# Performance work log

Hardware: AMD Instinct MI355X
Metric: run time of the kernel (lower is better)

The kernel has to match this reference:

```python
import jax, jax.numpy as jnp
import numpy as np

B, P, O, C = 32, 65536, 32, 2
THRESH = 0.35
VAR = (0.1, 0.2)
LOC_W, LANDM_W = 2.0, 1.0
ALPHA, GAMMA = 0.25, 1.5
EPS = 1e-7


def setup_inputs():
    key = jax.random.key(0)
    k = jax.random.split(key, 8)
    loc_data = jax.random.normal(k[0], (B, P, 4), jnp.float32) * 0.1
    conf_data = jax.random.normal(k[1], (B, P, C), jnp.float32)
    landm_data = jax.random.normal(k[2], (B, P, 10), jnp.float32) * 0.1
    # priors in center form (cx, cy, w, h)
    cxcy = jax.random.uniform(k[3], (P, 2), minval=0.05, maxval=0.95)
    wh = jax.random.uniform(k[4], (P, 2), minval=0.02, maxval=0.3)
    priors = jnp.concatenate([cxcy, wh], axis=-1).astype(jnp.float32)
    # targets [B, O, 15]: corner box (4) + 5 landmarks (10) + label (1, in {-1, +1})
    xy1 = jax.random.uniform(k[5], (B, O, 2), minval=0.0, maxval=0.7)
    bwh = jax.random.uniform(k[6], (B, O, 2), minval=0.05, maxval=0.25)
    boxes = jnp.concatenate([xy1, xy1 + bwh], axis=-1)
    landms = jnp.tile(xy1 + bwh * 0.5, (1, 1, 5))
    labels = (jax.random.randint(k[7], (B, O, 1), 0, 2) * 2 - 1).astype(jnp.float32)
    targets = jnp.concatenate([boxes, landms, labels], axis=-1)
    return {"loc_data": loc_data, "conf_data": conf_data, "landm_data": landm_data,
            "priors": priors, "targets": targets}


def point_form(pr):  # (cx,cy,w,h) -> (x1,y1,x2,y2)
    return jnp.concatenate([pr[:, :2] - pr[:, 2:] / 2, pr[:, :2] + pr[:, 2:] / 2], -1)


def pairwise_iou(a, b):  # a [O,4], b [P,4] corner form -> [O,P]
    lt = jnp.maximum(a[:, None, :2], b[None, :, :2])
    rb = jnp.minimum(a[:, None, 2:], b[None, :, 2:])
    whd = jnp.clip(rb - lt, 0.0)
    inter = whd[..., 0] * whd[..., 1]
    area_a = ((a[:, 2] - a[:, 0]) * (a[:, 3] - a[:, 1]))[:, None]
    area_b = ((b[:, 2] - b[:, 0]) * (b[:, 3] - b[:, 1]))[None, :]
    return inter / (area_a + area_b - inter)


def encode_landm(matched, priors):  # matched [P,10], priors [P,4] center form
    m = matched.reshape(P, 5, 2)
    g = (m - priors[:, None, :2]) / (VAR[0] * priors[:, None, 2:])
    return g.reshape(P, 10)


def match_one(truths, landms, labels, priors_pf, priors):
    ov = pairwise_iou(truths, priors_pf)                       # [O,P]
    best_prior_idx = jnp.argmax(ov, axis=1)                    # [O] best prior per gt
    best_truth_overlap = ov.max(axis=0)                        # [P]
    best_truth_idx = jnp.argmax(ov, axis=0)                    # [P]
    # ensure every gt keeps its best prior
    best_truth_overlap = best_truth_overlap.at[best_prior_idx].set(2.0)
    best_truth_idx = best_truth_idx.at[best_prior_idx].set(jnp.arange(truths.shape[0]))
    loc_t = truths[best_truth_idx]                             # [P,4] matched gt boxes (corner)
    conf = jnp.where(best_truth_overlap < THRESH, 0.0, labels[best_truth_idx])
    landm_t = encode_landm(landms[best_truth_idx], priors)     # [P,10]
    return loc_t, conf, landm_t


def decode(loc, priors):  # SSD center-form decode -> corner boxes
    xy = priors[..., :2] + loc[..., :2] * VAR[0] * priors[..., 2:]
    wh = priors[..., 2:] * jnp.exp(loc[..., 2:] * VAR[1])
    return jnp.concatenate([xy - wh / 2, xy + wh / 2], -1)


def giou(b1, b2):  # elementwise GIoU, corner form
    area1 = (b1[..., 2] - b1[..., 0]) * (b1[..., 3] - b1[..., 1])
    area2 = (b2[..., 2] - b2[..., 0]) * (b2[..., 3] - b2[..., 1])
    iw = jnp.clip(jnp.minimum(b1[..., 2], b2[..., 2]) - jnp.maximum(b1[..., 0], b2[..., 0]), 0.0)
    ih = jnp.clip(jnp.minimum(b1[..., 3], b2[..., 3]) - jnp.maximum(b1[..., 1], b2[..., 1]), 0.0)
    inter = iw * ih
    union = area1 + area2 - inter
    iou = inter / (union + EPS)
    ew = jnp.maximum(b1[..., 2], b2[..., 2]) - jnp.minimum(b1[..., 0], b2[..., 0])
    eh = jnp.maximum(b1[..., 3], b2[..., 3]) - jnp.minimum(b1[..., 1], b2[..., 1])
    enc = ew * eh
    return iou - (enc - union) / (enc + EPS)


def smooth_l1(x):
    ax = jnp.abs(x)
    return jnp.where(ax < 1.0, 0.5 * x * x, ax - 0.5)


def reference(loc_data, conf_data, landm_data, priors, targets):
    # matching uses detached (.data) priors/targets in the original
    priors_c = jax.lax.stop_gradient(priors)
    targets_c = jax.lax.stop_gradient(targets)
    truths, landms, labels = targets_c[..., :4], targets_c[..., 4:14], targets_c[..., 14]
    priors_pf = point_form(priors_c)
    loc_t, conf_raw, landm_t = jax.vmap(match_one, in_axes=(0, 0, 0, None, None))(
        truths, landms, labels, priors_pf, priors_c)  # [B,P,4],[B,P],[B,P,10]

    # landmark loss on pos1 = conf > 0 (label +1: face with landmarks)
    pos1 = conf_raw > 0
    N1 = jnp.maximum(pos1.sum().astype(jnp.float32), 1.0)
    loss_landm = (smooth_l1(landm_data - landm_t).sum(-1) * pos1).sum() * LANDM_W

    # loc GIoU loss on pos = conf != 0
    pos = conf_raw != 0
    conf_t = pos.astype(jnp.int32)  # conf_t[pos] = 1, background 0
    dec = decode(loc_data, priors_c[None])  # [B,P,4]
    loss_l = jnp.where(pos, 1.0 - giou(dec, loc_t), 0.0).sum() * LOC_W

    # focal loss over all B*P anchors (size_average=False -> sum)
    logp = jax.nn.log_softmax(conf_data, axis=-1)
    logp_t = jnp.take_along_axis(logp, conf_t[..., None], axis=-1)[..., 0]
    p_t = jnp.exp(logp_t)
    loss_c = (-ALPHA * (1.0 - p_t) ** GAMMA * logp_t).sum()

    # original normalizes loss_l and loss_c by num_pos_landm sum (N), landm by N1 (==N)
    N = N1
    return (loss_l / N, loss_c / N, loss_landm / N1)
```

## Files before the change

### kernel.cpp

```cpp
#include <hip/hip_runtime.h>
#include <cstdint>

#define B_ 32
#define P_ 65536
#define O_ 32
#define GX_ 64
#define KC_ 4
#define NXCD_ 8
#define NCELL_ 16
#define NC_ (NCELL_ * NCELL_)
#define HB_ 32
#define PPH_ (P_ / (HB_ * 256))
#define MARGIN_ 0.1501f
#define THRESH_ 0.35f
#define VAR0 0.1f
#define VAR1 0.2f
#define EPS_ 1e-7f
#define ALPHA_ 0.25f

struct WSHdr {
  unsigned long long gkey[B_ * O_];
  float4 part[GX_ * B_];
  double corr[B_][4];
  unsigned blkcnt[HB_ * NC_];
  unsigned blkbase[HB_ * NC_];
  unsigned cellid[P_];
  unsigned idx_sorted[P_];
  float4 priors_sorted[P_];
};

__device__ __forceinline__ float frcp(float x) { return __builtin_amdgcn_rcpf(x); }

template <int CTRL>
__device__ __forceinline__ float dpp_fmax(float v) {
  int s = __builtin_amdgcn_update_dpp(0, __float_as_int(v), CTRL, 0xF, 0xF, true);
  return fmaxf(v, __int_as_float(s));
}
template <int CTRL>
__device__ __forceinline__ unsigned dpp_umax(unsigned v) {
  unsigned u = (unsigned)__builtin_amdgcn_update_dpp(0, (int)v, CTRL, 0xF, 0xF, true);
  return u > v ? u : v;
}

__device__ __forceinline__ float focal_term(float2 cf, bool pos) {
  float mx = fmaxf(cf.x, cf.y);
  float lse = mx + __logf(1.f + __expf(-fabsf(cf.x - cf.y)));
  float logpt = (pos ? cf.y : cf.x) - lse;
  float pt = __expf(logpt);
  float om = 1.f - pt;
  return -ALPHA_ * om * sqrtf(om) * logpt;
}

__device__ __forceinline__ float giou_term(float4 pr, float4 loc,
                                           float b2x1, float b2y1,
                                           float b2x2, float b2y2) {
  float dx = pr.x + loc.x * VAR0 * pr.z;
  float dy = pr.y + loc.y * VAR0 * pr.w;
  float dw = pr.z * __expf(loc.z * VAR1);
  float dh = pr.w * __expf(loc.w * VAR1);
  float b1x1 = dx - dw * 0.5f, b1y1 = dy - dh * 0.5f;
  float b1x2 = dx + dw * 0.5f, b1y2 = dy + dh * 0.5f;
  float a1 = (b1x2 - b1x1) * (b1y2 - b1y1);
  float a2 = (b2x2 - b2x1) * (b2y2 - b2y1);
  float iw = fmaxf(fminf(b1x2, b2x2) - fmaxf(b1x1, b2x1), 0.f);
  float ih = fmaxf(fminf(b1y2, b2y2) - fmaxf(b1y1, b2y1), 0.f);
  float inter = iw * ih;
  float uni = a1 + a2 - inter;
  float iou = inter * frcp(uni + EPS_);
  float ew = fmaxf(b1x2, b2x2) - fminf(b1x1, b2x1);
  float eh = fmaxf(b1y2, b2y2) - fminf(b1y1, b2y1);
  float enc = ew * eh;
  float g = iou - (enc - uni) * frcp(enc + EPS_);
  return 1.f - g;
}

__device__ __forceinline__ float landm_term(float4 pr,
                                            const float* __restrict__ lmrow,
                                            const float* __restrict__ tlm_row) {
  float rw = frcp(VAR0 * pr.z);
  float rh = frcp(VAR0 * pr.w);
  float llm = 0.f;
  #pragma unroll
  for (int q = 0; q < 5; ++q) {
    float2 d = *reinterpret_cast<const float2*>(lmrow + q * 2);
    float ex = d.x - (tlm_row[2 * q] - pr.x) * rw;
    float ey = d.y - (tlm_row[2 * q + 1] - pr.y) * rh;
    float ax = fabsf(ex), ay = fabsf(ey);
    llm += (ax < 1.f) ? 0.5f * ex * ex : ax - 0.5f;
    llm += (ay < 1.f) ? 0.5f * ey * ey : ay - 0.5f;
  }
  return llm;
}


__global__ __launch_bounds__(256) void k_init2(WSHdr* ws) {
  const int t = blockIdx.x * 256 + threadIdx.x;
  if (t < B_ * O_) ws->gkey[t] = 0xFFFFFFFFull;
}

__global__ __launch_bounds__(256) void k_hist(const float* __restrict__ priors,
                                              WSHdr* __restrict__ ws) {
  __shared__ unsigned lh[NC_];
  const int tid = threadIdx.x;
  lh[tid] = 0u;
  __syncthreads();
  const int pb0 = blockIdx.x * (256 * PPH_);
  #pragma unroll
  for (int i = 0; i < PPH_; ++i) {
    const int p = pb0 + i * 256 + tid;
    float4 pr = reinterpret_cast<const float4*>(priors)[p];
    int cx = min(NCELL_ - 1, max(0, (int)(pr.x * (float)NCELL_)));
    int cy = min(NCELL_ - 1, max(0, (int)(pr.y * (float)NCELL_)));
    unsigned c = (unsigned)(cy * NCELL_ + cx);
    ws->cellid[p] = c;
    atomicAdd(&lh[c], 1u);
  }
  __syncthreads();
  ws->blkcnt[blockIdx.x * NC_ + tid] = lh[tid];
}

__global__ __launch_bounds__(256) void k_scan2(WSHdr* ws) {
  __shared__ unsigned s[NC_];
  const int c = threadIdx.x;
  unsigned tot = 0;
  for (int blk = 0; blk < HB_; ++blk) tot += ws->blkcnt[blk * NC_ + c];
  s[c] = tot;
  __syncthreads();
  for (int off = 1; off < NC_; off <<= 1) {
    unsigned t = (c >= off) ? s[c - off] : 0u;
    __syncthreads();
    s[c] += t;
    __syncthreads();
  }
  unsigned run = s[c] - tot;
  for (int blk = 0; blk < HB_; ++blk) {
    ws->blkbase[blk * NC_ + c] = run;
    run += ws->blkcnt[blk * NC_ + c];
  }
}

__global__ __launch_bounds__(256) void k_scatter2(const float* __restrict__ priors,
                                                  WSHdr* __restrict__ ws) {
  __shared__ unsigned lcur[NC_];
  const int tid = threadIdx.x;
  lcur[tid] = ws->blkbase[blockIdx.x * NC_ + tid];
  __syncthreads();
  const int pb0 = blockIdx.x * (256 * PPH_);
  #pragma unroll
  for (int i = 0; i < PPH_; ++i) {
    const int p = pb0 + i * 256 + tid;
    unsigned c = ws->cellid[p];
    unsigned slot = atomicAdd(&lcur[c], 1u);
    ws->idx_sorted[slot] = (unsigned)p;
    ws->priors_sorted[slot] = reinterpret_cast<const float4*>(priors)[p];
  }
}

__global__ __launch_bounds__(256) void k_fused2(const float* __restrict__ loc_data,
                                                const float* __restrict__ conf_data,
                                                const float* __restrict__ landm_data,
                                                const float* __restrict__ targets,
                                                WSHdr* __restrict__ ws) {
  __shared__ float tsh[O_][4];
  __shared__ float tlbl[O_];
  __shared__ float tlm[O_][10];
  __shared__ unsigned long long kq[O_][17];
  __shared__ float4 wsum[4];
  const int bid = blockIdx.x;
  const int xcd = bid & (NXCD_ - 1);
  const int j = bid >> 3;
  const int b = xcd * (B_ / NXCD_) + (j & (B_ / NXCD_ - 1));
  const int bx = j >> 2;
  const int tid = threadIdx.x;
  const int lane = tid & 63, wid = tid >> 6;
  if (tid < O_) {
    const float* trow = targets + ((size_t)b * O_ + tid) * 15;
    tsh[tid][0] = trow[0]; tsh[tid][1] = trow[1];
    tsh[tid][2] = trow[2]; tsh[tid][3] = trow[3];
    #pragma unroll
    for (int k = 0; k < 10; ++k) tlm[tid][k] = trow[4 + k];
    tlbl[tid] = trow[14];
  }
  for (int i = tid; i < O_ * 17; i += 256) ((unsigned long long*)kq)[i] = 0ull;
  __syncthreads();

  const int slot0 = bx * 1024 + tid * KC_;
  float4 pr[KC_];
  float px1[KC_], py1[KC_], px2[KC_], py2[KC_], pa[KC_], bov[KC_];
  int bidx[KC_];
  unsigned pinv[KC_];
  uint4 opv = *reinterpret_cast<const uint4*>(&ws->idx_sorted[slot0]);
  pinv[0] = 0xFFFFFFFFu - opv.x; pinv[1] = 0xFFFFFFFFu - opv.y;
  pinv[2] = 0xFFFFFFFFu - opv.z; pinv[3] = 0xFFFFFFFFu - opv.w;
  float mnx = 1e9f, mxx = -1e9f, mny = 1e9f, mxy = -1e9f;
  #pragma unroll
  for (int k = 0; k < KC_; ++k) {
    pr[k] = ws->priors_sorted[slot0 + k];
    px1[k] = pr[k].x - pr[k].z * 0.5f; py1[k] = pr[k].y - pr[k].w * 0.5f;
    px2[k] = pr[k].x + pr[k].z * 0.5f; py2[k] = pr[k].y + pr[k].w * 0.5f;
    pa[k] = (px2[k] - px1[k]) * (py2[k] - py1[k]);
    bov[k] = 0.f; bidx[k] = 0;
    mnx = fminf(mnx, pr[k].x); mxx = fmaxf(mxx, pr[k].x);
    mny = fminf(mny, pr[k].y); mxy = fmaxf(mxy, pr[k].y);
  }
  #pragma unroll
  for (int i = 1; i < 64; i <<= 1) {
    mnx = fminf(mnx, __shfl_xor(mnx, i));
    mxx = fmaxf(mxx, __shfl_xor(mxx, i));
    mny = fminf(mny, __shfl_xor(mny, i));
    mxy = fmaxf(mxy, __shfl_xor(mxy, i));
  }

  const float* __restrict__ tb = targets + (size_t)b * O_ * 15;
  for (int o = 0; o < O_; ++o) {
    const float x1 = tb[o * 15 + 0], y1 = tb[o * 15 + 1];
    const float x2 = tb[o * 15 + 2], y2 = tb[o * 15 + 3];
    bool hit = (x1 - MARGIN_ <= mxx) && (x2 + MARGIN_ >= mnx) &&
               (y1 - MARGIN_ <= mxy) && (y2 + MARGIN_ >= mny);
    if (hit) {
      const float ta = (x2 - x1) * (y2 - y1);
      float tiou = 0.f;
      unsigned tinv = 0u;
      #pragma unroll
      for (int k = 0; k < KC_; ++k) {
        float iw = fmaxf(fminf(x2, px2[k]) - fmaxf(x1, px1[k]), 0.f);
        float ih = fmaxf(fminf(y2, py2[k]) - fmaxf(y1, py1[k]), 0.f);
        float inter = iw * ih;
        float iou = inter * frcp(ta + pa[k] - inter);
        if (iou > bov[k]) { bov[k] = iou; bidx[k] = o; }
        if (iou > tiou || (iou == tiou && pinv[k] > tinv)) {
          tiou = iou; tinv = pinv[k];
        }
      }
      float m = tiou;
      m = dpp_fmax<0x128>(m);
      m = dpp_fmax<0x124>(m);
      m = dpp_fmax<0x122>(m);
      m = dpp_fmax<0x121>(m);
      unsigned cand = (tiou == m) ? tinv : 0u;
      cand = dpp_umax<0x128>(cand);
      cand = dpp_umax<0x124>(cand);
      cand = dpp_umax<0x122>(cand);
      cand = dpp_umax<0x121>(cand);
      if ((lane & 15) == 0)
        kq[o][wid * 4 + (lane >> 4)] =
            ((unsigned long long)__float_as_uint(m) << 32) |
            (unsigned long long)cand;
    }
  }

  float vx = 0.f, vy = 0.f, vz = 0.f, vw = 0.f;
  #pragma unroll
  for (int k = 0; k < KC_; ++k) {
    const unsigned p = 0xFFFFFFFFu - pinv[k];
    const size_t bp = (size_t)b * P_ + p;
    const float ov = bov[k];
    const int idx = bidx[k];
    const bool pos = !(ov < THRESH_);
    const bool pos1 = pos && (tlbl[idx] > 0.f);
    float2 cf = reinterpret_cast<const float2*>(conf_data)[bp];
    vy += focal_term(cf, pos);
    if (pos) {
      float4 loc = reinterpret_cast<const float4*>(loc_data)[bp];
      vx += giou_term(pr[k], loc, tsh[idx][0], tsh[idx][1], tsh[idx][2], tsh[idx][3]);
      if (pos1) {
        vw += 1.f;
        vz += landm_term(pr[k], landm_data + bp * 10, &tlm[idx][0]);
      }
    }
  }

  __syncthreads();
  if (tid < O_) {
    unsigned long long best = kq[tid][0];
    #pragma unroll
    for (int s = 1; s < 16; ++s) {
      unsigned long long v = kq[tid][s];
      if (v > best) best = v;
    }
    atomicMax(&ws->gkey[(size_t)b * O_ + tid], best);
  }

  #pragma unroll
  for (int i = 32; i > 0; i >>= 1) {
    vx += __shfl_xor(vx, i);
    vy += __shfl_xor(vy, i);
    vz += __shfl_xor(vz, i);
    vw += __shfl_xor(vw, i);
  }
  if (lane == 0) wsum[wid] = make_float4(vx, vy, vz, vw);
  __syncthreads();
  if (tid == 0) {
    float sx = 0.f, sy = 0.f, sz = 0.f, sw = 0.f;
    #pragma unroll
    for (int w = 0; w < 4; ++w) {
      sx += wsum[w].x; sy += wsum[w].y; sz += wsum[w].z; sw += wsum[w].w;
    }
    ws->part[(size_t)b * GX_ + bx] = make_float4(sx, sy, sz, sw);
  }
}

__global__ __launch_bounds__(64) void k_fix(const float* __restrict__ loc_data,
                                            const float* __restrict__ conf_data,
                                            const float* __restrict__ landm_data,
                                            const float* __restrict__ priors,
                                            const float* __restrict__ targets,
                                            WSHdr* __restrict__ ws) {
  __shared__ float tsh[O_][5];
  __shared__ float tlbl[O_];
  __shared__ float tlm[O_][10];
  const int b = blockIdx.x;
  const int tid = threadIdx.x;
  if (tid < O_) {
    const float* trow = targets + ((size_t)b * O_ + tid) * 15;
    float x1 = trow[0], y1 = trow[1], x2 = trow[2], y2 = trow[3];
    tsh[tid][0] = x1; tsh[tid][1] = y1; tsh[tid][2] = x2; tsh[tid][3] = y2;
    tsh[tid][4] = (x2 - x1) * (y2 - y1);
    #pragma unroll
    for (int k = 0; k < 10; ++k) tlm[tid][k] = trow[4 + k];
    tlbl[tid] = trow[14];
  }
  __syncthreads();

  unsigned fp = 0xFFFFFFFFu;
  if (tid < O_)
    fp = 0xFFFFFFFFu - (unsigned)(ws->gkey[(size_t)b * O_ + tid] & 0xFFFFFFFFull);
  bool alive = tid < O_;
  for (int j2 = 0; j2 < O_; ++j2) {
    unsigned f2 = __shfl(fp, j2, 64);
    if (j2 > tid && f2 == fp) alive = false;
  }

  float dll = 0.f, dlc = 0.f, dllm = 0.f, dn1 = 0.f;
  if (alive) {
    const int p = (int)fp;
    const size_t bp = (size_t)b * P_ + p;
    float4 pr = reinterpret_cast<const float4*>(priors)[p];
    float px1 = pr.x - pr.z * 0.5f, py1 = pr.y - pr.w * 0.5f;
    float px2 = pr.x + pr.z * 0.5f, py2 = pr.y + pr.w * 0.5f;
    float pa = (px2 - px1) * (py2 - py1);
    float bov = 0.f;
    int bidx = 0;
    for (int o = 0; o < O_; ++o) {
      const float x1 = tsh[o][0], y1 = tsh[o][1], x2 = tsh[o][2], y2 = tsh[o][3];
      const float ta = tsh[o][4];
      float iw = fmaxf(fminf(x2, px2) - fmaxf(x1, px1), 0.f);
      float ih = fmaxf(fminf(y2, py2) - fmaxf(y1, py1), 0.f);
      float inter = iw * ih;
      float iou = inter * frcp(ta + pa - inter);
      if (iou > bov) { bov = iou; bidx = o; }
    }
    float2 cf = reinterpret_cast<const float2*>(conf_data)[bp];
    float4 loc = reinterpret_cast<const float4*>(loc_data)[bp];
    const float* lmrow = landm_data + bp * 10;
    {
      const bool pos = !(bov < THRESH_);
      const bool pos1 = pos && (tlbl[bidx] > 0.f);
      dlc -= focal_term(cf, pos);
      if (pos) {
        dll -= giou_term(pr, loc, tsh[bidx][0], tsh[bidx][1], tsh[bidx][2], tsh[bidx][3]);
        if (pos1) {
          dn1 -= 1.f;
          dllm -= landm_term(pr, lmrow, &tlm[bidx][0]);
        }
      }
    }
    {
      const int idx = tid;
      const bool pos1 = tlbl[idx] > 0.f;
      dlc += focal_term(cf, true);
      dll += giou_term(pr, loc, tsh[idx][0], tsh[idx][1], tsh[idx][2], tsh[idx][3]);
      if (pos1) {
        dn1 += 1.f;
        dllm += landm_term(pr, lmrow, &tlm[idx][0]);
      }
    }
  }
  #pragma unroll
  for (int i = 32; i > 0; i >>= 1) {
    dll += __shfl_xor(dll, i);
    dlc += __shfl_xor(dlc, i);
    dllm += __shfl_xor(dllm, i);
    dn1 += __shfl_xor(dn1, i);
  }
  if (tid == 0) {
    ws->corr[b][0] = (double)dll;
    ws->corr[b][1] = (double)dlc;
    ws->corr[b][2] = (double)dllm;
    ws->corr[b][3] = (double)dn1;
  }
}

__global__ __launch_bounds__(256) void k_final(const WSHdr* __restrict__ ws,
                                               float* __restrict__ out) {
  __shared__ double sh[4][4];
  const int tid = threadIdx.x;
  double sx = 0.0, sy = 0.0, sz = 0.0, sw = 0.0;
  for (int i = tid; i < GX_ * B_; i += 256) {
    float4 v = ws->part[i];
    sx += v.x; sy += v.y; sz += v.z; sw += v.w;
  }
  if (tid < B_) {
    sx += ws->corr[tid][0];
    sy += ws->corr[tid][1];
    sz += ws->corr[tid][2];
    sw += ws->corr[tid][3];
  }
  #pragma unroll
  for (int i = 32; i > 0; i >>= 1) {
    sx += __shfl_xor(sx, i);
    sy += __shfl_xor(sy, i);
    sz += __shfl_xor(sz, i);
    sw += __shfl_xor(sw, i);
  }
  const int wave = tid >> 6, lane = tid & 63;
  if (lane == 0) { sh[wave][0] = sx; sh[wave][1] = sy; sh[wave][2] = sz; sh[wave][3] = sw; }
  __syncthreads();
  if (tid == 0) {
    double ax = 0, ay = 0, az = 0, aw = 0;
    #pragma unroll
    for (int w = 0; w < 4; ++w) { ax += sh[w][0]; ay += sh[w][1]; az += sh[w][2]; aw += sh[w][3]; }
    double n1 = aw < 1.0 ? 1.0 : aw;
    out[0] = (float)(2.0 * ax / n1);
    out[1] = (float)(ay / n1);
    out[2] = (float)(az / n1);
  }
}

extern "C" void kernel_launch(void* const* d_in, const int* in_sizes, int n_in,
                              void* d_out, int out_size, void* d_ws, size_t ws_size,
                              hipStream_t stream) {
  (void)in_sizes; (void)n_in; (void)out_size; (void)ws_size;
  const float* loc     = (const float*)d_in[0];
  const float* conf    = (const float*)d_in[1];
  const float* landm   = (const float*)d_in[2];
  const float* priors  = (const float*)d_in[3];
  const float* targets = (const float*)d_in[4];
  WSHdr* ws = (WSHdr*)d_ws;
  float* out = (float*)d_out;

  hipLaunchKernelGGL(k_init2, dim3(4), dim3(256), 0, stream, ws);
  hipLaunchKernelGGL(k_hist, dim3(HB_), dim3(256), 0, stream, priors, ws);
  hipLaunchKernelGGL(k_scan2, dim3(1), dim3(256), 0, stream, ws);
  hipLaunchKernelGGL(k_scatter2, dim3(HB_), dim3(256), 0, stream, priors, ws);
  hipLaunchKernelGGL(k_fused2, dim3(GX_ * B_), dim3(256), 0, stream,
                     loc, conf, landm, targets, ws);
  hipLaunchKernelGGL(k_fix, dim3(B_), dim3(64), 0, stream,
                     loc, conf, landm, priors, targets, ws);
  hipLaunchKernelGGL(k_final, dim3(1), dim3(256), 0, stream, ws, out);
}
```

Before: 71.57 us.

## Fold init and scan kernels into hist/scatter and remap fused block order

Removes the separate init and single-block scan launches: block 0 of the histogram kernel now initializes gkey, and each scatter block recomputes the cell-wise totals, the exclusive scan and its own per-block prefix from blkcnt. This cuts two small kernel launches and their serialization bubbles, at the cost of redundant scan work in each of the 32 scatter blocks. The fused kernel's block-to-(batch, chunk) mapping also changes so that consecutive blocks on an XCD walk contiguous chunks of one batch, aiming at better cache locality.

```diff
diff --git a/kernel.cpp b/kernel.cpp
--- a/kernel.cpp
+++ b/kernel.cpp
@@ -93,16 +93,14 @@
 }
 
 
-__global__ __launch_bounds__(256) void k_init2(WSHdr* ws) {
-  const int t = blockIdx.x * 256 + threadIdx.x;
-  if (t < B_ * O_) ws->gkey[t] = 0xFFFFFFFFull;
-}
-
 __global__ __launch_bounds__(256) void k_hist(const float* __restrict__ priors,
                                               WSHdr* __restrict__ ws) {
   __shared__ unsigned lh[NC_];
   const int tid = threadIdx.x;
   lh[tid] = 0u;
+  if (blockIdx.x == 0) {
+    for (int i = tid; i < B_ * O_; i += 256) ws->gkey[i] = 0xFFFFFFFFull;
+  }
   __syncthreads();
   const int pb0 = blockIdx.x * (256 * PPH_);
   #pragma unroll
@@ -119,31 +117,26 @@
   ws->blkcnt[blockIdx.x * NC_ + tid] = lh[tid];
 }
 
-__global__ __launch_bounds__(256) void k_scan2(WSHdr* ws) {
-  __shared__ unsigned s[NC_];
-  const int c = threadIdx.x;
-  unsigned tot = 0;
-  for (int blk = 0; blk < HB_; ++blk) tot += ws->blkcnt[blk * NC_ + c];
-  s[c] = tot;
-  __syncthreads();
-  for (int off = 1; off < NC_; off <<= 1) {
-    unsigned t = (c >= off) ? s[c - off] : 0u;
-    __syncthreads();
-    s[c] += t;
-    __syncthreads();
-  }
-  unsigned run = s[c] - tot;
-  for (int blk = 0; blk < HB_; ++blk) {
-    ws->blkbase[blk * NC_ + c] = run;
-    run += ws->blkcnt[blk * NC_ + c];
-  }
-}
-
 __global__ __launch_bounds__(256) void k_scatter2(const float* __restrict__ priors,
                                                   WSHdr* __restrict__ ws) {
   __shared__ unsigned lcur[NC_];
+  __shared__ unsigned s[NC_];
   const int tid = threadIdx.x;
-  lcur[tid] = ws->blkbase[blockIdx.x * NC_ + tid];
+  unsigned totc = 0u, pre = 0u;
+  for (int blk = 0; blk < HB_; ++blk) {
+    unsigned v = ws->blkcnt[blk * NC_ + tid];
+    if (blk < (int)blockIdx.x) pre += v;
+    totc += v;
+  }
+  s[tid] = totc;
+  __syncthreads();
+  for (int off = 1; off < NC_; off <<= 1) {
+    unsigned t = (tid >= off) ? s[tid - off] : 0u;
+    __syncthreads();
+    s[tid] += t;
+    __syncthreads();
+  }
+  lcur[tid] = (s[tid] - totc) + pre;
   __syncthreads();
   const int pb0 = blockIdx.x * (256 * PPH_);
   #pragma unroll
@@ -169,8 +162,8 @@
   const int bid = blockIdx.x;
   const int xcd = bid & (NXCD_ - 1);
   const int j = bid >> 3;
-  const int b = xcd * (B_ / NXCD_) + (j & (B_ / NXCD_ - 1));
-  const int bx = j >> 2;
+  const int b = xcd * (B_ / NXCD_) + (j >> 6);
+  const int bx = j & 63;
   const int tid = threadIdx.x;
   const int lane = tid & 63, wid = tid >> 6;
   if (tid < O_) {
@@ -439,9 +432,7 @@
   WSHdr* ws = (WSHdr*)d_ws;
   float* out = (float*)d_out;
 
-  hipLaunchKernelGGL(k_init2, dim3(4), dim3(256), 0, stream, ws);
   hipLaunchKernelGGL(k_hist, dim3(HB_), dim3(256), 0, stream, priors, ws);
-  hipLaunchKernelGGL(k_scan2, dim3(1), dim3(256), 0, stream, ws);
   hipLaunchKernelGGL(k_scatter2, dim3(HB_), dim3(256), 0, stream, priors, ws);
   hipLaunchKernelGGL(k_fused2, dim3(GX_ * B_), dim3(256), 0, stream,
                      loc, conf, landm, targets, ws);
```

New measurement: 71.55 us. About the same (-0.0%).
